# Kernel optimization log

Hardware: AMD Instinct MI355X
Metric: run time of the kernel (lower is better)

## Reference

```python
import jax, jax.numpy as jnp
import numpy as np

N_USER = 27094
M_SPOT = 42852
N_EDGE = 2_000_000
D_FEAT = 128


def setup_inputs() -> dict:
    key = jax.random.key(0)
    k1, k2, k3, k4 = jax.random.split(key, 4)
    spot_x = jax.random.normal(k1, (M_SPOT, D_FEAT), dtype=jnp.float32)
    user_x = jax.random.normal(k2, (N_USER, D_FEAT), dtype=jnp.float32)
    u_idx = jax.random.randint(k3, (N_EDGE,), 0, N_USER, dtype=jnp.int32)
    s_idx = jax.random.randint(k4, (N_EDGE,), 0, M_SPOT, dtype=jnp.int32)
    user_spot = jnp.stack([u_idx, s_idx], axis=0)  # [2, E]
    return {"spot_x": spot_x, "user_x": user_x, "user_spot": user_spot}


def reference(spot_x, user_x, user_spot):
    u = user_spot[0]  # [E] user index per edge
    s = user_spot[1]  # [E] spot index per edge
    # symmetric GCN normalization: 1/sqrt(deg_u * deg_s) per edge
    user_deg = jnp.bincount(u, length=N_USER)
    spot_deg = jnp.bincount(s, length=M_SPOT)
    div = jnp.sqrt((user_deg[u] * spot_deg[s]).astype(spot_x.dtype))[:, None]  # [E,1]
    # spot -> user aggregation
    source_spot = spot_x[s] / div                                   # [E, D]
    user_out = jax.ops.segment_sum(source_spot, u, num_segments=N_USER)
    # user -> spot aggregation
    source_user = user_x[u] / div                                   # [E, D]
    spot_out = jax.ops.segment_sum(source_user, s, num_segments=M_SPOT)
    return (spot_out, user_out)
```

## Files before the change

kernel.cpp:

```cpp
#include <hip/hip_runtime.h>
#include <stdint.h>


#define NPB_LOG2 6
#define NPB 64
#define MAXB 768
#define PART_CHUNK 2048
#define BH_CHUNK 16384
#define SORT_CAP 8192
#define RCAP 4096

__device__ __forceinline__ ushort f2bf(float f) {
    uint32_t u = __float_as_uint(f);
    return (ushort)((u + 0x7fffu + ((u >> 16) & 1u)) >> 16);
}

__global__ __launch_bounds__(256) void bhist_kernel(
        const int* __restrict__ u, const int* __restrict__ s, int E,
        int nbu, int nbs, int* __restrict__ bd) {
    __shared__ int hist[2 * MAXB];
    const int tid = threadIdx.x;
    const int nb = nbu + nbs;
    const int beg = blockIdx.x * BH_CHUNK;
    const int end = min(beg + BH_CHUNK, E);
    for (int b = tid; b < nb; b += 256) hist[b] = 0;
    __syncthreads();
    for (int i = beg + tid; i < end; i += 256) {
        atomicAdd(&hist[u[i] >> NPB_LOG2], 1);
        atomicAdd(&hist[nbu + (s[i] >> NPB_LOG2)], 1);
    }
    __syncthreads();
    for (int b = tid; b < nb; b += 256) {
        int h = hist[b];
        if (h) atomicAdd(&bd[b], h);
    }
}

__global__ __launch_bounds__(1024) void scan2_kernel(
        const int* __restrict__ bd, int nbu, int nbs,
        int* __restrict__ buoff, int* __restrict__ bsoff,
        int* __restrict__ gcu, int* __restrict__ gcs) {
    __shared__ int wsums[16];
    __shared__ int total;
    const int tid = threadIdx.x, lane = tid & 63, wid = tid >> 6;
    const int n   = blockIdx.x ? nbs : nbu;
    const int* in = blockIdx.x ? (bd + nbu) : bd;
    int* out = blockIdx.x ? bsoff : buoff;
    int* gc  = blockIdx.x ? gcs   : gcu;
    int v = (tid < n) ? in[tid] : 0;
    int x = v;
#pragma unroll
    for (int d = 1; d < 64; d <<= 1) {
        int t = __shfl_up(x, d);
        if (lane >= d) x += t;
    }
    if (lane == 63) wsums[wid] = x;
    __syncthreads();
    if (tid == 0) {
        int run = 0;
#pragma unroll
        for (int w = 0; w < 16; ++w) { int t = wsums[w]; wsums[w] = run; run += t; }
        total = run;
    }
    __syncthreads();
    int excl = wsums[wid] + (x - v);
    if (tid < n) { out[tid] = excl; gc[tid] = excl; }
    if (tid == 0) out[n] = total;
}

__global__ void convert2_kernel(const float* __restrict__ spot_x,
                                const float* __restrict__ user_x,
                                const float* __restrict__ isd_s,
                                const float* __restrict__ isd_u,
                                ushort* __restrict__ xbs, ushort* __restrict__ xbu,
                                int M, int N) {
    int idx = blockIdx.x * blockDim.x + threadIdx.x;
    if (idx >= ((M + N) << 6)) return;
    int row = idx >> 6, c = idx & 63;
    const float* x; float w; ushort* xb;
    if (row < M) { x = spot_x + ((size_t)row << 7); w = isd_s[row]; xb = xbs + ((size_t)row << 7); }
    else { row -= M; x = user_x + ((size_t)row << 7); w = isd_u[row]; xb = xbu + ((size_t)row << 7); }
    ushort2 o;
    o.x = f2bf(x[c] * w);
    o.y = f2bf(x[c + 64] * w);
    *reinterpret_cast<ushort2*>(xb + 2 * c) = o;
}

__global__ void convert_kernel(const float* __restrict__ x, const float* __restrict__ isd,
                               ushort* __restrict__ xb, int n_rows) {
    int idx = blockIdx.x * blockDim.x + threadIdx.x;
    if (idx >= (n_rows << 6)) return;
    int row = idx >> 6, c = idx & 63;
    float w = isd[row];
    const float* xr = x + ((size_t)row << 7);
    ushort2 o;
    o.x = f2bf(xr[c] * w);
    o.y = f2bf(xr[c + 64] * w);
    *reinterpret_cast<ushort2*>(xb + ((size_t)row << 7) + 2 * c) = o;
}

__global__ __launch_bounds__(256) void part2_kernel(
        const int* __restrict__ u, const int* __restrict__ s, int E,
        int nbu, int nbs, int* __restrict__ gcu, int* __restrict__ gcs,
        uint32_t* __restrict__ outU, uint32_t* __restrict__ outS) {
    __shared__ int histU[MAXB], loffU[MAXB], gbaseU[MAXB], curU[MAXB];
    __shared__ int histS[MAXB], loffS[MAXB], gbaseS[MAXB], curS[MAXB];
    __shared__ int wsum[4];
    __shared__ uint32_t sbufU[PART_CHUNK];
    __shared__ uint32_t sbufS[PART_CHUNK];
    const int tid = threadIdx.x;
    const int lane = tid & 63;
    const int wid = tid >> 6;
    const int beg = blockIdx.x * PART_CHUNK;
    const int end = min(beg + PART_CHUNK, E);
    const int cnt_total = end - beg;
    for (int b = tid; b < nbu; b += 256) histU[b] = 0;
    for (int b = tid; b < nbs; b += 256) histS[b] = 0;
    __syncthreads();
    for (int i = beg + tid; i < end; i += 256) {
        atomicAdd(&histU[u[i] >> NPB_LOG2], 1);
        atomicAdd(&histS[s[i] >> NPB_LOG2], 1);
    }
    __syncthreads();
    for (int dir = 0; dir < 2; ++dir) {
        int nb = dir ? nbs : nbu;
        int* hist = dir ? histS : histU;
        int* loff = dir ? loffS : loffU;
        int b0 = tid * 3;
        int h0 = (b0 + 0 < nb) ? hist[b0 + 0] : 0;
        int h1 = (b0 + 1 < nb) ? hist[b0 + 1] : 0;
        int h2 = (b0 + 2 < nb) ? hist[b0 + 2] : 0;
        int tsum = h0 + h1 + h2;
        int x = tsum;
#pragma unroll
        for (int d = 1; d < 64; d <<= 1) {
            int t = __shfl_up(x, d);
            if (lane >= d) x += t;
        }
        if (lane == 63) wsum[wid] = x;
        __syncthreads();
        if (tid == 0) {
            int run = 0;
#pragma unroll
            for (int w = 0; w < 4; ++w) { int t = wsum[w]; wsum[w] = run; run += t; }
        }
        __syncthreads();
        int base = wsum[wid] + (x - tsum);
        if (b0 + 0 < nb) loff[b0 + 0] = base;
        if (b0 + 1 < nb) loff[b0 + 1] = base + h0;
        if (b0 + 2 < nb) loff[b0 + 2] = base + h0 + h1;
        __syncthreads();
    }
    for (int b = tid; b < nbu; b += 256) {
        curU[b] = loffU[b];
        int c = histU[b];
        gbaseU[b] = c > 0 ? atomicAdd(&gcu[b], c) : 0;
    }
    for (int b = tid; b < nbs; b += 256) {
        curS[b] = loffS[b];
        int c = histS[b];
        gbaseS[b] = c > 0 ? atomicAdd(&gcs[b], c) : 0;
    }
    __syncthreads();
    for (int i = beg + tid; i < end; i += 256) {
        int uu = u[i], ss = s[i];
        int lu = atomicAdd(&curU[uu >> NPB_LOG2], 1);
        sbufU[lu] = ((uint32_t)uu << 16) | (uint32_t)ss;
        int ls = atomicAdd(&curS[ss >> NPB_LOG2], 1);
        sbufS[ls] = ((uint32_t)ss << 16) | (uint32_t)uu;
    }
    __syncthreads();
    for (int k = tid; k < cnt_total; k += 256) {
        uint32_t p = sbufU[k];
        int b = (int)(p >> (16 + NPB_LOG2));
        outU[gbaseU[b] + (k - loffU[b])] = p;
        uint32_t q = sbufS[k];
        int b2 = (int)(q >> (16 + NPB_LOG2));
        outS[gbaseS[b2] + (k - loffS[b2])] = q;
    }
}

__global__ __launch_bounds__(256) void bdeg2_kernel(
        const uint32_t* __restrict__ bufU, const uint32_t* __restrict__ bufS,
        const int* __restrict__ buoff, const int* __restrict__ bsoff, int nbu,
        float* __restrict__ isd_u, float* __restrict__ isd_s, int N, int M) {
    __shared__ int hist[NPB];
    const int tid = threadIdx.x;
    const int b = blockIdx.x;
    const uint32_t* buf; const int* boff; float* isd; int n_rows; int bb;
    if (b < nbu) { buf = bufU; boff = buoff; isd = isd_u; n_rows = N; bb = b; }
    else         { buf = bufS; boff = bsoff; isd = isd_s; n_rows = M; bb = b - nbu; }
    const int jbeg = boff[bb];
    const int cnt = boff[bb + 1] - jbeg;
    if (tid < NPB) hist[tid] = 0;
    __syncthreads();
    for (int k = tid; k < cnt; k += 256)
        atomicAdd(&hist[(buf[jbeg + k] >> 16) & (NPB - 1)], 1);
    __syncthreads();
    if (tid < NPB) {
        int node = (bb << NPB_LOG2) + tid;
        if (node < n_rows) {
            int h = hist[tid];
            isd[node] = h > 0 ? rsqrtf((float)h) : 0.f;
        }
    }
}

__global__ __launch_bounds__(512) void fscan3_kernel(
        const ushort* __restrict__ xb, const uint32_t* __restrict__ buf,
        const int* __restrict__ boff, const float* __restrict__ isd,
        float* __restrict__ out, int split) {
    __shared__ ushort srt[RCAP];
    __shared__ int hist[NPB];
    __shared__ int scur[NPB];
    const int tid = threadIdx.x;
    const int bucket = blockIdx.x / split;
    const int sub = blockIdx.x - bucket * split;
    const int jb = boff[bucket];
    const int cnt = boff[bucket + 1] - jb;
    if (cnt <= 0) return;
    const int sbeg = jb + (int)((long long)cnt * sub / split);
    const int send = jb + (int)((long long)cnt * (sub + 1) / split);
    const int scnt = send - sbeg;
    if (scnt <= 0) return;
    const int wid = tid >> 6, lane = tid & 63;
    const int rowbase = bucket << NPB_LOG2;

#define ROWX(sv) (*reinterpret_cast<const uint32_t*>( \
        xb + (((size_t)(sv)) << 7) + (lane << 1)))
#define UPX(rv) __uint_as_float((rv) << 16)
#define UPY(rv) __uint_as_float((rv) & 0xffff0000u)

    if (scnt <= RCAP) {
        if (tid < NPB) hist[tid] = 0;
        __syncthreads();
        uint32_t ereg[8];
#pragma unroll
        for (int k = 0; k < 8; ++k) {
            int idx = sbeg + (k << 9) + tid;
            if (idx < send) {
                ereg[k] = buf[idx];
                atomicAdd(&hist[(ereg[k] >> 16) & (NPB - 1)], 1);
            } else ereg[k] = 0u;
        }
        __syncthreads();
        if (tid < NPB) {
            int h = hist[tid];
            int x = h;
#pragma unroll
            for (int d = 1; d < 64; d <<= 1) {
                int t = __shfl_up(x, d);
                if (tid >= d) x += t;
            }
            scur[tid] = x - h;
        }
        __syncthreads();
#pragma unroll
        for (int k = 0; k < 8; ++k) {
            int idx = sbeg + (k << 9) + tid;
            if (idx < send) {
                uint32_t p = ereg[k];
                int slot = atomicAdd(&scur[(p >> 16) & (NPB - 1)], 1);
                srt[slot] = (ushort)p;
            }
        }
        __syncthreads();
        for (int ld = wid; ld < NPB; ld += 8) {
            const int deg = hist[ld];
            if (!deg) continue;
            const int off0 = scur[ld] - deg;
            float ax = 0.f, ay = 0.f;
            int j = 0;
            if (deg >= 16) {
                ushort c0 = srt[off0+0], c1 = srt[off0+1], c2 = srt[off0+2], c3 = srt[off0+3],
                       c4 = srt[off0+4], c5 = srt[off0+5], c6 = srt[off0+6], c7 = srt[off0+7];
                uint32_t r0 = ROWX(c0), r1 = ROWX(c1), r2 = ROWX(c2), r3 = ROWX(c3),
                         r4 = ROWX(c4), r5 = ROWX(c5), r6 = ROWX(c6), r7 = ROWX(c7);
                for (j = 8; j + 8 <= deg; j += 8) {
                    const int q = off0 + j;
                    ushort n0 = srt[q+0], n1 = srt[q+1], n2 = srt[q+2], n3 = srt[q+3],
                           n4 = srt[q+4], n5 = srt[q+5], n6 = srt[q+6], n7 = srt[q+7];
                    uint32_t s0 = ROWX(n0), s1 = ROWX(n1), s2 = ROWX(n2), s3 = ROWX(n3),
                             s4 = ROWX(n4), s5 = ROWX(n5), s6 = ROWX(n6), s7 = ROWX(n7);
                    ax += ((UPX(r0) + UPX(r1)) + (UPX(r2) + UPX(r3)))
                        + ((UPX(r4) + UPX(r5)) + (UPX(r6) + UPX(r7)));
                    ay += ((UPY(r0) + UPY(r1)) + (UPY(r2) + UPY(r3)))
                        + ((UPY(r4) + UPY(r5)) + (UPY(r6) + UPY(r7)));
                    r0 = s0; r1 = s1; r2 = s2; r3 = s3;
                    r4 = s4; r5 = s5; r6 = s6; r7 = s7;
                }
                ax += ((UPX(r0) + UPX(r1)) + (UPX(r2) + UPX(r3)))
                    + ((UPX(r4) + UPX(r5)) + (UPX(r6) + UPX(r7)));
                ay += ((UPY(r0) + UPY(r1)) + (UPY(r2) + UPY(r3)))
                    + ((UPY(r4) + UPY(r5)) + (UPY(r6) + UPY(r7)));
            }
            for (; j < deg; ++j) {
                uint32_t r = ROWX(srt[off0 + j]);
                ax += UPX(r); ay += UPY(r);
            }
            const float w = isd[rowbase + ld];
            const size_t ro = ((size_t)(rowbase + ld)) << 7;
            unsafeAtomicAdd(out + ro + lane,      ax * w);
            unsafeAtomicAdd(out + ro + 64 + lane, ay * w);
        }
    } else {
        const int cs = (scnt + 7) >> 3;
        const int beg = sbeg + wid * cs;
        const int end = min(beg + cs, send);
        if (beg >= end) return;
        float ax = 0.f, ay = 0.f;
        int curd = (int)(buf[beg] >> 16);
        for (int k = beg; k < end; ++k) {
            uint32_t p = buf[k];
            int d_ = (int)(p >> 16);
            if (d_ != curd) {
                float w_ = isd[curd];
                unsafeAtomicAdd(out + ((size_t)curd << 7) + lane, ax * w_);
                unsafeAtomicAdd(out + ((size_t)curd << 7) + 64 + lane, ay * w_);
                ax = 0.f; ay = 0.f; curd = d_;
            }
            uint32_t r = ROWX((ushort)p);
            ax += UPX(r); ay += UPY(r);
        }
        float w_ = isd[curd];
        unsafeAtomicAdd(out + ((size_t)curd << 7) + lane, ax * w_);
        unsafeAtomicAdd(out + ((size_t)curd << 7) + 64 + lane, ay * w_);
    }
#undef UPY
#undef UPX
#undef ROWX
}


__global__ __launch_bounds__(256) void bdeg_kernel(
        const uint32_t* __restrict__ buf, const int* __restrict__ boff,
        float* __restrict__ isd, int n_rows) {
    __shared__ int hist[NPB];
    const int tid = threadIdx.x;
    const int jbeg = boff[blockIdx.x];
    const int cnt = boff[blockIdx.x + 1] - jbeg;
    if (tid < NPB) hist[tid] = 0;
    __syncthreads();
    for (int k = tid; k < cnt; k += 256)
        atomicAdd(&hist[(buf[jbeg + k] >> 16) & (NPB - 1)], 1);
    __syncthreads();
    if (tid < NPB) {
        int node = (blockIdx.x << NPB_LOG2) + tid;
        if (node < n_rows) {
            int h = hist[tid];
            isd[node] = h > 0 ? rsqrtf((float)h) : 0.f;
        }
    }
}

__global__ __launch_bounds__(512) void fscan_kernel(
        const ushort* __restrict__ xb, const uint32_t* __restrict__ buf,
        const int* __restrict__ boff, float* __restrict__ isd_out,
        float* __restrict__ out, int n_rows) {
    __shared__ uint32_t sorted[SORT_CAP];
    __shared__ int hist[NPB];
    __shared__ int scur[NPB];
    __shared__ float isdl[NPB];
    const int tid = threadIdx.x;
    const int jbeg = boff[blockIdx.x];
    const int cnt = boff[blockIdx.x + 1] - jbeg;
    if (cnt <= 0) {
        if (tid < NPB) {
            int node = (blockIdx.x << NPB_LOG2) + tid;
            if (node < n_rows) isd_out[node] = 0.f;
        }
        return;
    }
    const bool fits = (cnt <= SORT_CAP);
    if (tid < NPB) hist[tid] = 0;
    __syncthreads();
    for (int k = tid; k < cnt; k += 512)
        atomicAdd(&hist[(buf[jbeg + k] >> 16) & (NPB - 1)], 1);
    __syncthreads();
    if (tid < NPB) {
        int h = hist[tid];
        int x = h;
#pragma unroll
        for (int d = 1; d < 64; d <<= 1) {
            int t = __shfl_up(x, d);
            if (tid >= d) x += t;
        }
        scur[tid] = x - h;
        float iv = h > 0 ? rsqrtf((float)h) : 0.f;
        isdl[tid] = iv;
        int node = (blockIdx.x << NPB_LOG2) + tid;
        if (node < n_rows) isd_out[node] = iv;
    }
    __syncthreads();
    if (fits) {
        for (int k = tid; k < cnt; k += 512) {
            uint32_t p = buf[jbeg + k];
            int slot = atomicAdd(&scur[(p >> 16) & (NPB - 1)], 1);
            sorted[slot] = p;
        }
    }
    __syncthreads();
    const int wid = tid >> 6, lane = tid & 63;
    const int cs = (cnt + 7) >> 3;
    const int beg = wid * cs;
    const int end = min(beg + cs, cnt);
    if (beg >= end) return;

#define QLD(i) (fits ? sorted[i] : buf[jbeg + (i)])
#define ROW(pv) (*reinterpret_cast<const uint32_t*>( \
        xb + (((size_t)((pv) & 0xffffu)) << 7) + (lane << 1)))
#define UPX(rv) __uint_as_float((rv) << 16)
#define UPY(rv) __uint_as_float((rv) & 0xffff0000u)
    float ax = 0.f, ay = 0.f;
    int curd = (int)(QLD(beg) >> 16);
    for (int k = beg; k < end; ++k) {
        uint32_t p = QLD(k);
        int d_ = (int)(p >> 16);
        if (d_ != curd) {
            float w_ = isdl[curd & (NPB - 1)];
            unsafeAtomicAdd(out + ((size_t)curd << 7) + lane, ax * w_);
            unsafeAtomicAdd(out + ((size_t)curd << 7) + 64 + lane, ay * w_);
            ax = 0.f; ay = 0.f; curd = d_;
        }
        uint32_t r = ROW(p);
        ax += UPX(r); ay += UPY(r);
    }
    float w_ = isdl[curd & (NPB - 1)];
    unsafeAtomicAdd(out + ((size_t)curd << 7) + lane, ax * w_);
    unsafeAtomicAdd(out + ((size_t)curd << 7) + 64 + lane, ay * w_);
#undef UPY
#undef UPX
#undef ROW
#undef QLD
}


__global__ void deg_kernel(const int* __restrict__ u, const int* __restrict__ s,
                           int E, int* __restrict__ udeg, int* __restrict__ sdeg) {
    int i = blockIdx.x * blockDim.x + threadIdx.x;
    if (i < E) {
        atomicAdd(&udeg[u[i]], 1);
        atomicAdd(&sdeg[s[i]], 1);
    }
}

__global__ void init_isd_kernel(const int* __restrict__ udeg, const int* __restrict__ sdeg,
                                float* __restrict__ isd_u, float* __restrict__ isd_s,
                                int n_user, int m_spot) {
    int i = blockIdx.x * blockDim.x + threadIdx.x;
    if (i < n_user) { int d = udeg[i]; isd_u[i] = d > 0 ? rsqrtf((float)d) : 0.f; }
    if (i < m_spot) { int d = sdeg[i]; isd_s[i] = d > 0 ? rsqrtf((float)d) : 0.f; }
}

__global__ __launch_bounds__(256) void scatter_kernel(const float* __restrict__ spot_x,
                                                      const float* __restrict__ user_x,
                                                      const int* __restrict__ u,
                                                      const int* __restrict__ s, int E,
                                                      const float* __restrict__ isd_u,
                                                      const float* __restrict__ isd_s,
                                                      float* __restrict__ spot_out,
                                                      float* __restrict__ user_out) {
    const int lane = threadIdx.x & 63;
    const int e = blockIdx.x * 4 + (threadIdx.x >> 6);
    if (e >= E) return;
    const int uu = u[e], ss = s[e];
    const float w = isd_u[uu] * isd_s[ss];
    const float2 sv = *reinterpret_cast<const float2*>(spot_x + (size_t)ss * 128 + lane * 2);
    const float2 uv = *reinterpret_cast<const float2*>(user_x + (size_t)uu * 128 + lane * 2);
    atomicAdd(&user_out[(size_t)uu * 128 + lane * 2 + 0], sv.x * w);
    atomicAdd(&user_out[(size_t)uu * 128 + lane * 2 + 1], sv.y * w);
    atomicAdd(&spot_out[(size_t)ss * 128 + lane * 2 + 0], uv.x * w);
    atomicAdd(&spot_out[(size_t)ss * 128 + lane * 2 + 1], uv.y * w);
}

static inline char* align256(char* p) {
    return (char*)(((uintptr_t)p + 255u) & ~(uintptr_t)255u);
}

extern "C" void kernel_launch(void* const* d_in, const int* in_sizes, int n_in,
                              void* d_out, int out_size, void* d_ws, size_t ws_size,
                              hipStream_t stream) {
    const float* spot_x = (const float*)d_in[0];
    const float* user_x = (const float*)d_in[1];
    const int*   edges  = (const int*)d_in[2];
    const int M = in_sizes[0] / 128;
    const int N = in_sizes[1] / 128;
    const int E = in_sizes[2] / 2;
    const int* u = edges;
    const int* s = edges + E;
    float* spot_out = (float*)d_out;
    float* user_out = (float*)d_out + (size_t)M * 128;

    const int nbu = (N + NPB - 1) / NPB;
    const int nbs = (M + NPB - 1) / NPB;
    const int nm = (N > M) ? N : M;
    const int gpart = (E + PART_CHUNK - 1) / PART_CHUNK;

    char* ws = (char*)d_ws;
    float*    isd_u = (float*)ws; ws = align256(ws + sizeof(float) * (size_t)N);
    float*    isd_s = (float*)ws; ws = align256(ws + sizeof(float) * (size_t)M);
    int*      bd    = (int*)ws;   ws = align256(ws + sizeof(int) * (size_t)(nbu + nbs));
    int*      buoff = (int*)ws;   ws = align256(ws + sizeof(int) * (size_t)(nbu + 1));
    int*      bsoff = (int*)ws;   ws = align256(ws + sizeof(int) * (size_t)(nbs + 1));
    int*      gcu   = (int*)ws;   ws = align256(ws + sizeof(int) * (size_t)nbu);
    int*      gcs   = (int*)ws;   ws = align256(ws + sizeof(int) * (size_t)nbs);
    uint32_t* bufU  = (uint32_t*)ws; ws = align256(ws + sizeof(uint32_t) * (size_t)E);
    uint32_t* bufS  = (uint32_t*)ws; ws = align256(ws + sizeof(uint32_t) * (size_t)E);
    ushort*   xbs   = (ushort*)ws;
    ushort*   xbu   = (ushort*)align256((char*)xbs + sizeof(ushort) * ((size_t)M * 128));
    size_t tierA_needed = (size_t)((char*)xbu - (char*)d_ws)
                        + sizeof(ushort) * ((size_t)N * 128);
    size_t tierB_needed = (size_t)((char*)xbs - (char*)d_ws)
                        + sizeof(ushort) * ((size_t)nm * 128);

    if (tierB_needed <= ws_size && nbu <= MAXB && nbs <= MAXB) {
        hipMemsetAsync(bd, 0, sizeof(int) * (size_t)(nbu + nbs), stream);
        hipMemsetAsync(d_out, 0, sizeof(float) * (size_t)out_size, stream);
        bhist_kernel<<<(E + BH_CHUNK - 1) / BH_CHUNK, 256, 0, stream>>>(
            u, s, E, nbu, nbs, bd);
        scan2_kernel<<<2, 1024, 0, stream>>>(bd, nbu, nbs, buoff, bsoff, gcu, gcs);
        part2_kernel<<<gpart, 256, 0, stream>>>(u, s, E, nbu, nbs, gcu, gcs, bufU, bufS);
        if (tierA_needed <= ws_size) {
            bdeg2_kernel<<<nbu + nbs, 256, 0, stream>>>(
                bufU, bufS, buoff, bsoff, nbu, isd_u, isd_s, N, M);
            convert2_kernel<<<(((M + N) << 6) + 255) / 256, 256, 0, stream>>>(
                spot_x, user_x, isd_s, isd_u, xbs, xbu, M, N);
            int splitU = 2048 / nbu; if (splitU < 1) splitU = 1; if (splitU > 16) splitU = 16;
            int splitS = 2048 / nbs; if (splitS < 1) splitS = 1; if (splitS > 16) splitS = 16;
            fscan3_kernel<<<nbu * splitU, 512, 0, stream>>>(
                xbs, bufU, buoff, isd_u, user_out, splitU);
            fscan3_kernel<<<nbs * splitS, 512, 0, stream>>>(
                xbu, bufS, bsoff, isd_s, spot_out, splitS);
        } else {
            ushort* xb = xbs;
            bdeg_kernel<<<nbs, 256, 0, stream>>>(bufS, bsoff, isd_s, M);
            convert_kernel<<<((M << 6) + 255) / 256, 256, 0, stream>>>(spot_x, isd_s, xb, M);
            fscan_kernel<<<nbu, 512, 0, stream>>>(xb, bufU, buoff, isd_u, user_out, N);
            convert_kernel<<<((N << 6) + 255) / 256, 256, 0, stream>>>(user_x, isd_u, xb, N);
            fscan_kernel<<<nbs, 512, 0, stream>>>(xb, bufS, bsoff, isd_s, spot_out, M);
        }
        return;
    }

    {
        char* w2 = (char*)d_ws;
        int*   udeg2  = (int*)w2;   w2 += sizeof(int) * (size_t)N;
        int*   sdeg2  = (int*)w2;   w2 += sizeof(int) * (size_t)M;
        float* isd_u2 = (float*)w2; w2 += sizeof(float) * (size_t)N;
        float* isd_s2 = (float*)w2; w2 += sizeof(float) * (size_t)M;
        if ((size_t)(w2 - (char*)d_ws) <= ws_size) {
            hipMemsetAsync(udeg2, 0, sizeof(int) * (size_t)(N + M), stream);
            deg_kernel<<<(E + 255) / 256, 256, 0, stream>>>(u, s, E, udeg2, sdeg2);
            init_isd_kernel<<<(nm + 255) / 256, 256, 0, stream>>>(
                udeg2, sdeg2, isd_u2, isd_s2, N, M);
            hipMemsetAsync(d_out, 0, sizeof(float) * (size_t)out_size, stream);
            scatter_kernel<<<((size_t)E + 3) / 4, 256, 0, stream>>>(
                spot_x, user_x, u, s, E, isd_u2, isd_s2, spot_out, user_out);
        }
    }
}
```

Measured before the change: 293.6 us.

## Fully sort bucket edges in place, then gather with fixed-chunk wave scans

```diff
diff --git a/kernel.cpp b/kernel.cpp
--- a/kernel.cpp
+++ b/kernel.cpp
@@ -8,7 +8,7 @@
 #define PART_CHUNK 2048
 #define BH_CHUNK 16384
 #define SORT_CAP 8192
-#define RCAP 4096
+#define CSCAN_CH 256
 
 __device__ __forceinline__ ushort f2bf(float f) {
     uint32_t u = __float_as_uint(f);
@@ -180,202 +180,28 @@
     }
 }
 
-__global__ __launch_bounds__(256) void bdeg2_kernel(
-        const uint32_t* __restrict__ bufU, const uint32_t* __restrict__ bufS,
+__global__ __launch_bounds__(256) void bsort3b_kernel(
+        uint32_t* __restrict__ bufU, uint32_t* __restrict__ bufS,
         const int* __restrict__ buoff, const int* __restrict__ bsoff, int nbu,
         float* __restrict__ isd_u, float* __restrict__ isd_s, int N, int M) {
+    __shared__ uint32_t stage[SORT_CAP];
     __shared__ int hist[NPB];
+    __shared__ int cur[NPB];
     const int tid = threadIdx.x;
     const int b = blockIdx.x;
-    const uint32_t* buf; const int* boff; float* isd; int n_rows; int bb;
+    uint32_t* buf; const int* boff; float* isd; int n_rows; int bb;
     if (b < nbu) { buf = bufU; boff = buoff; isd = isd_u; n_rows = N; bb = b; }
     else         { buf = bufS; boff = bsoff; isd = isd_s; n_rows = M; bb = b - nbu; }
     const int jbeg = boff[bb];
     const int cnt = boff[bb + 1] - jbeg;
-    if (tid < NPB) hist[tid] = 0;
-    __syncthreads();
-    for (int k = tid; k < cnt; k += 256)
-        atomicAdd(&hist[(buf[jbeg + k] >> 16) & (NPB - 1)], 1);
-    __syncthreads();
-    if (tid < NPB) {
-        int node = (bb << NPB_LOG2) + tid;
-        if (node < n_rows) {
-            int h = hist[tid];
-            isd[node] = h > 0 ? rsqrtf((float)h) : 0.f;
-        }
-    }
-}
-
-__global__ __launch_bounds__(512) void fscan3_kernel(
-        const ushort* __restrict__ xb, const uint32_t* __restrict__ buf,
-        const int* __restrict__ boff, const float* __restrict__ isd,
-        float* __restrict__ out, int split) {
-    __shared__ ushort srt[RCAP];
-    __shared__ int hist[NPB];
-    __shared__ int scur[NPB];
-    const int tid = threadIdx.x;
-    const int bucket = blockIdx.x / split;
-    const int sub = blockIdx.x - bucket * split;
-    const int jb = boff[bucket];
-    const int cnt = boff[bucket + 1] - jb;
-    if (cnt <= 0) return;
-    const int sbeg = jb + (int)((long long)cnt * sub / split);
-    const int send = jb + (int)((long long)cnt * (sub + 1) / split);
-    const int scnt = send - sbeg;
-    if (scnt <= 0) return;
-    const int wid = tid >> 6, lane = tid & 63;
-    const int rowbase = bucket << NPB_LOG2;
-
-#define ROWX(sv) (*reinterpret_cast<const uint32_t*>( \
-        xb + (((size_t)(sv)) << 7) + (lane << 1)))
-#define UPX(rv) __uint_as_float((rv) << 16)
-#define UPY(rv) __uint_as_float((rv) & 0xffff0000u)
-
-    if (scnt <= RCAP) {
-        if (tid < NPB) hist[tid] = 0;
-        __syncthreads();
-        uint32_t ereg[8];
-#pragma unroll
-        for (int k = 0; k < 8; ++k) {
-            int idx = sbeg + (k << 9) + tid;
-            if (idx < send) {
-                ereg[k] = buf[idx];
-                atomicAdd(&hist[(ereg[k] >> 16) & (NPB - 1)], 1);
-            } else ereg[k] = 0u;
-        }
-        __syncthreads();
-        if (tid < NPB) {
-            int h = hist[tid];
-            int x = h;
-#pragma unroll
-            for (int d = 1; d < 64; d <<= 1) {
-                int t = __shfl_up(x, d);
-                if (tid >= d) x += t;
-            }
-            scur[tid] = x - h;
-        }
-        __syncthreads();
-#pragma unroll
-        for (int k = 0; k < 8; ++k) {
-            int idx = sbeg + (k << 9) + tid;
-            if (idx < send) {
-                uint32_t p = ereg[k];
-                int slot = atomicAdd(&scur[(p >> 16) & (NPB - 1)], 1);
-                srt[slot] = (ushort)p;
-            }
-        }
-        __syncthreads();
-        for (int ld = wid; ld < NPB; ld += 8) {
-            const int deg = hist[ld];
-            if (!deg) continue;
-            const int off0 = scur[ld] - deg;
-            float ax = 0.f, ay = 0.f;
-            int j = 0;
-            if (deg >= 16) {
-                ushort c0 = srt[off0+0], c1 = srt[off0+1], c2 = srt[off0+2], c3 = srt[off0+3],
-                       c4 = srt[off0+4], c5 = srt[off0+5], c6 = srt[off0+6], c7 = srt[off0+7];
-                uint32_t r0 = ROWX(c0), r1 = ROWX(c1), r2 = ROWX(c2), r3 = ROWX(c3),
-                         r4 = ROWX(c4), r5 = ROWX(c5), r6 = ROWX(c6), r7 = ROWX(c7);
-                for (j = 8; j + 8 <= deg; j += 8) {
-                    const int q = off0 + j;
-                    ushort n0 = srt[q+0], n1 = srt[q+1], n2 = srt[q+2], n3 = srt[q+3],
-                           n4 = srt[q+4], n5 = srt[q+5], n6 = srt[q+6], n7 = srt[q+7];
-                    uint32_t s0 = ROWX(n0), s1 = ROWX(n1), s2 = ROWX(n2), s3 = ROWX(n3),
-                             s4 = ROWX(n4), s5 = ROWX(n5), s6 = ROWX(n6), s7 = ROWX(n7);
-                    ax += ((UPX(r0) + UPX(r1)) + (UPX(r2) + UPX(r3)))
-                        + ((UPX(r4) + UPX(r5)) + (UPX(r6) + UPX(r7)));
-                    ay += ((UPY(r0) + UPY(r1)) + (UPY(r2) + UPY(r3)))
-                        + ((UPY(r4) + UPY(r5)) + (UPY(r6) + UPY(r7)));
-                    r0 = s0; r1 = s1; r2 = s2; r3 = s3;
-                    r4 = s4; r5 = s5; r6 = s6; r7 = s7;
-                }
-                ax += ((UPX(r0) + UPX(r1)) + (UPX(r2) + UPX(r3)))
-                    + ((UPX(r4) + UPX(r5)) + (UPX(r6) + UPX(r7)));
-                ay += ((UPY(r0) + UPY(r1)) + (UPY(r2) + UPY(r3)))
-                    + ((UPY(r4) + UPY(r5)) + (UPY(r6) + UPY(r7)));
-            }
-            for (; j < deg; ++j) {
-                uint32_t r = ROWX(srt[off0 + j]);
-                ax += UPX(r); ay += UPY(r);
-            }
-            const float w = isd[rowbase + ld];
-            const size_t ro = ((size_t)(rowbase + ld)) << 7;
-            unsafeAtomicAdd(out + ro + lane,      ax * w);
-            unsafeAtomicAdd(out + ro + 64 + lane, ay * w);
-        }
-    } else {
-        const int cs = (scnt + 7) >> 3;
-        const int beg = sbeg + wid * cs;
-        const int end = min(beg + cs, send);
-        if (beg >= end) return;
-        float ax = 0.f, ay = 0.f;
-        int curd = (int)(buf[beg] >> 16);
-        for (int k = beg; k < end; ++k) {
-            uint32_t p = buf[k];
-            int d_ = (int)(p >> 16);
-            if (d_ != curd) {
-                float w_ = isd[curd];
-                unsafeAtomicAdd(out + ((size_t)curd << 7) + lane, ax * w_);
-                unsafeAtomicAdd(out + ((size_t)curd << 7) + 64 + lane, ay * w_);
-                ax = 0.f; ay = 0.f; curd = d_;
-            }
-            uint32_t r = ROWX((ushort)p);
-            ax += UPX(r); ay += UPY(r);
-        }
-        float w_ = isd[curd];
-        unsafeAtomicAdd(out + ((size_t)curd << 7) + lane, ax * w_);
-        unsafeAtomicAdd(out + ((size_t)curd << 7) + 64 + lane, ay * w_);
-    }
-#undef UPY
-#undef UPX
-#undef ROWX
-}
-
-
-__global__ __launch_bounds__(256) void bdeg_kernel(
-        const uint32_t* __restrict__ buf, const int* __restrict__ boff,
-        float* __restrict__ isd, int n_rows) {
-    __shared__ int hist[NPB];
-    const int tid = threadIdx.x;
-    const int jbeg = boff[blockIdx.x];
-    const int cnt = boff[blockIdx.x + 1] - jbeg;
-    if (tid < NPB) hist[tid] = 0;
-    __syncthreads();
-    for (int k = tid; k < cnt; k += 256)
-        atomicAdd(&hist[(buf[jbeg + k] >> 16) & (NPB - 1)], 1);
-    __syncthreads();
-    if (tid < NPB) {
-        int node = (blockIdx.x << NPB_LOG2) + tid;
-        if (node < n_rows) {
-            int h = hist[tid];
-            isd[node] = h > 0 ? rsqrtf((float)h) : 0.f;
-        }
-    }
-}
-
-__global__ __launch_bounds__(512) void fscan_kernel(
-        const ushort* __restrict__ xb, const uint32_t* __restrict__ buf,
-        const int* __restrict__ boff, float* __restrict__ isd_out,
-        float* __restrict__ out, int n_rows) {
-    __shared__ uint32_t sorted[SORT_CAP];
-    __shared__ int hist[NPB];
-    __shared__ int scur[NPB];
-    __shared__ float isdl[NPB];
-    const int tid = threadIdx.x;
-    const int jbeg = boff[blockIdx.x];
-    const int cnt = boff[blockIdx.x + 1] - jbeg;
-    if (cnt <= 0) {
-        if (tid < NPB) {
-            int node = (blockIdx.x << NPB_LOG2) + tid;
-            if (node < n_rows) isd_out[node] = 0.f;
-        }
-        return;
-    }
     const bool fits = (cnt <= SORT_CAP);
     if (tid < NPB) hist[tid] = 0;
     __syncthreads();
-    for (int k = tid; k < cnt; k += 512)
-        atomicAdd(&hist[(buf[jbeg + k] >> 16) & (NPB - 1)], 1);
+    for (int k = tid; k < cnt; k += 256) {
+        uint32_t p = buf[jbeg + k];
+        if (fits) stage[k] = p;
+        atomicAdd(&hist[(p >> 16) & (NPB - 1)], 1);
+    }
     __syncthreads();
     if (tid < NPB) {
         int h = hist[tid];
@@ -385,53 +211,91 @@
             int t = __shfl_up(x, d);
             if (tid >= d) x += t;
         }
-        scur[tid] = x - h;
-        float iv = h > 0 ? rsqrtf((float)h) : 0.f;
-        isdl[tid] = iv;
-        int node = (blockIdx.x << NPB_LOG2) + tid;
-        if (node < n_rows) isd_out[node] = iv;
+        cur[tid] = x - h;
+        int node = (bb << NPB_LOG2) + tid;
+        if (node < n_rows) isd[node] = h > 0 ? rsqrtf((float)h) : 0.f;
     }
     __syncthreads();
     if (fits) {
-        for (int k = tid; k < cnt; k += 512) {
-            uint32_t p = buf[jbeg + k];
-            int slot = atomicAdd(&scur[(p >> 16) & (NPB - 1)], 1);
-            sorted[slot] = p;
-        }
-    }
-    __syncthreads();
-    const int wid = tid >> 6, lane = tid & 63;
-    const int cs = (cnt + 7) >> 3;
-    const int beg = wid * cs;
-    const int end = min(beg + cs, cnt);
-    if (beg >= end) return;
-
-#define QLD(i) (fits ? sorted[i] : buf[jbeg + (i)])
+        for (int k = tid; k < cnt; k += 256) {
+            uint32_t p = stage[k];
+            int slot = atomicAdd(&cur[(p >> 16) & (NPB - 1)], 1);
+            buf[jbeg + slot] = p;
+        }
+    }
+}
+
+__global__ __launch_bounds__(256) void cscan_kernel(
+        const ushort* __restrict__ xb, const uint32_t* __restrict__ packed, int E,
+        const float* __restrict__ isd, float* __restrict__ out) {
+    const int lane = threadIdx.x & 63;
+    const int wave = (blockIdx.x << 2) + (threadIdx.x >> 6);
+    const int base = wave * CSCAN_CH;
+    if (base >= E) return;
+    const int n = min(CSCAN_CH, E - base);
+    const uint32_t* pp = packed + base;
+    float ax = 0.f, ay = 0.f;
+    int cur = (int)(pp[0] >> 16);
+
 #define ROW(pv) (*reinterpret_cast<const uint32_t*>( \
         xb + (((size_t)((pv) & 0xffffu)) << 7) + (lane << 1)))
 #define UPX(rv) __uint_as_float((rv) << 16)
 #define UPY(rv) __uint_as_float((rv) & 0xffff0000u)
-    float ax = 0.f, ay = 0.f;
-    int curd = (int)(QLD(beg) >> 16);
-    for (int k = beg; k < end; ++k) {
-        uint32_t p = QLD(k);
-        int d_ = (int)(p >> 16);
-        if (d_ != curd) {
-            float w_ = isdl[curd & (NPB - 1)];
-            unsafeAtomicAdd(out + ((size_t)curd << 7) + lane, ax * w_);
-            unsafeAtomicAdd(out + ((size_t)curd << 7) + 64 + lane, ay * w_);
-            ax = 0.f; ay = 0.f; curd = d_;
-        }
+#define FLUSH() do { float w_ = isd[cur];                                  \
+        unsafeAtomicAdd(out + ((size_t)cur << 7) + lane, ax * w_);         \
+        unsafeAtomicAdd(out + ((size_t)cur << 7) + 64 + lane, ay * w_);    \
+        ax = 0.f; ay = 0.f; } while (0)
+#define PROC(pv, rv) do { int d_ = (int)((pv) >> 16);                      \
+        if (d_ != cur) { FLUSH(); cur = d_; }                              \
+        ax += UPX(rv); ay += UPY(rv); } while (0)
+#define GRP8(Aa, Ab, r0, r1, r2, r3, r4, r5, r6, r7) do {                  \
+    if ((((Aa.x ^ Ab.w) >> 16) == 0) && ((int)(Aa.x >> 16) == cur)) {      \
+        float sx = ((UPX(r0) + UPX(r1)) + (UPX(r2) + UPX(r3)))             \
+                 + ((UPX(r4) + UPX(r5)) + (UPX(r6) + UPX(r7)));            \
+        float sy = ((UPY(r0) + UPY(r1)) + (UPY(r2) + UPY(r3)))             \
+                 + ((UPY(r4) + UPY(r5)) + (UPY(r6) + UPY(r7)));            \
+        ax += sx; ay += sy;                                                \
+    } else {                                                               \
+        PROC(Aa.x, r0); PROC(Aa.y, r1); PROC(Aa.z, r2); PROC(Aa.w, r3);    \
+        PROC(Ab.x, r4); PROC(Ab.y, r5); PROC(Ab.z, r6); PROC(Ab.w, r7);    \
+    } } while (0)
+
+    int k = 0;
+    if (n >= 24) {
+        uint4 P0a = *(const uint4*)(pp + 0),  P0b = *(const uint4*)(pp + 4);
+        uint4 P1a = *(const uint4*)(pp + 8),  P1b = *(const uint4*)(pp + 12);
+        uint32_t a0 = ROW(P0a.x), a1 = ROW(P0a.y), a2 = ROW(P0a.z), a3 = ROW(P0a.w),
+                 a4 = ROW(P0b.x), a5 = ROW(P0b.y), a6 = ROW(P0b.z), a7 = ROW(P0b.w);
+        uint4 P2a = *(const uint4*)(pp + 16), P2b = *(const uint4*)(pp + 20);
+        uint32_t b0 = ROW(P1a.x), b1 = ROW(P1a.y), b2 = ROW(P1a.z), b3 = ROW(P1a.w),
+                 b4 = ROW(P1b.x), b5 = ROW(P1b.y), b6 = ROW(P1b.z), b7 = ROW(P1b.w);
+        for (k = 24; k + 8 <= n; k += 8) {
+            uint4 P3a = *(const uint4*)(pp + k), P3b = *(const uint4*)(pp + k + 4);
+            uint32_t c0 = ROW(P2a.x), c1 = ROW(P2a.y), c2 = ROW(P2a.z), c3 = ROW(P2a.w),
+                     c4 = ROW(P2b.x), c5 = ROW(P2b.y), c6 = ROW(P2b.z), c7 = ROW(P2b.w);
+            GRP8(P0a, P0b, a0, a1, a2, a3, a4, a5, a6, a7);
+            P0a = P1a; P0b = P1b; P1a = P2a; P1b = P2b; P2a = P3a; P2b = P3b;
+            a0 = b0; a1 = b1; a2 = b2; a3 = b3; a4 = b4; a5 = b5; a6 = b6; a7 = b7;
+            b0 = c0; b1 = c1; b2 = c2; b3 = c3; b4 = c4; b5 = c5; b6 = c6; b7 = c7;
+        }
+        uint32_t c0 = ROW(P2a.x), c1 = ROW(P2a.y), c2 = ROW(P2a.z), c3 = ROW(P2a.w),
+                 c4 = ROW(P2b.x), c5 = ROW(P2b.y), c6 = ROW(P2b.z), c7 = ROW(P2b.w);
+        GRP8(P0a, P0b, a0, a1, a2, a3, a4, a5, a6, a7);
+        GRP8(P1a, P1b, b0, b1, b2, b3, b4, b5, b6, b7);
+        GRP8(P2a, P2b, c0, c1, c2, c3, c4, c5, c6, c7);
+    }
+    for (; k < n; ++k) {
+        uint32_t p = pp[k];
         uint32_t r = ROW(p);
-        ax += UPX(r); ay += UPY(r);
-    }
-    float w_ = isdl[curd & (NPB - 1)];
-    unsafeAtomicAdd(out + ((size_t)curd << 7) + lane, ax * w_);
-    unsafeAtomicAdd(out + ((size_t)curd << 7) + 64 + lane, ay * w_);
+        PROC(p, r);
+    }
+    FLUSH();
+#undef GRP8
+#undef PROC
+#undef FLUSH
 #undef UPY
 #undef UPX
 #undef ROW
-#undef QLD
 }
 
 
@@ -495,6 +359,7 @@
     const int nbs = (M + NPB - 1) / NPB;
     const int nm = (N > M) ? N : M;
     const int gpart = (E + PART_CHUNK - 1) / PART_CHUNK;
+    const int gscan = ((E + CSCAN_CH - 1) / CSCAN_CH + 3) / 4;
 
     char* ws = (char*)d_ws;
     float*    isd_u = (float*)ws; ws = align256(ws + sizeof(float) * (size_t)N);
@@ -520,24 +385,19 @@
             u, s, E, nbu, nbs, bd);
         scan2_kernel<<<2, 1024, 0, stream>>>(bd, nbu, nbs, buoff, bsoff, gcu, gcs);
         part2_kernel<<<gpart, 256, 0, stream>>>(u, s, E, nbu, nbs, gcu, gcs, bufU, bufS);
+        bsort3b_kernel<<<nbu + nbs, 256, 0, stream>>>(
+            bufU, bufS, buoff, bsoff, nbu, isd_u, isd_s, N, M);
         if (tierA_needed <= ws_size) {
-            bdeg2_kernel<<<nbu + nbs, 256, 0, stream>>>(
-                bufU, bufS, buoff, bsoff, nbu, isd_u, isd_s, N, M);
             convert2_kernel<<<(((M + N) << 6) + 255) / 256, 256, 0, stream>>>(
                 spot_x, user_x, isd_s, isd_u, xbs, xbu, M, N);
-            int splitU = 2048 / nbu; if (splitU < 1) splitU = 1; if (splitU > 16) splitU = 16;
-            int splitS = 2048 / nbs; if (splitS < 1) splitS = 1; if (splitS > 16) splitS = 16;
-            fscan3_kernel<<<nbu * splitU, 512, 0, stream>>>(
-                xbs, bufU, buoff, isd_u, user_out, splitU);
-            fscan3_kernel<<<nbs * splitS, 512, 0, stream>>>(
-                xbu, bufS, bsoff, isd_s, spot_out, splitS);
+            cscan_kernel<<<gscan, 256, 0, stream>>>(xbs, bufU, E, isd_u, user_out);
+            cscan_kernel<<<gscan, 256, 0, stream>>>(xbu, bufS, E, isd_s, spot_out);
         } else {
             ushort* xb = xbs;
-            bdeg_kernel<<<nbs, 256, 0, stream>>>(bufS, bsoff, isd_s, M);
             convert_kernel<<<((M << 6) + 255) / 256, 256, 0, stream>>>(spot_x, isd_s, xb, M);
-            fscan_kernel<<<nbu, 512, 0, stream>>>(xb, bufU, buoff, isd_u, user_out, N);
+            cscan_kernel<<<gscan, 256, 0, stream>>>(xb, bufU, E, isd_u, user_out);
             convert_kernel<<<((N << 6) + 255) / 256, 256, 0, stream>>>(user_x, isd_u, xb, N);
-            fscan_kernel<<<nbs, 512, 0, stream>>>(xb, bufS, bsoff, isd_s, spot_out, M);
+            cscan_kernel<<<gscan, 256, 0, stream>>>(xb, bufS, E, isd_s, spot_out);
         }
         return;
     }
```

New measurement: 238.3 us. 1.23x faster.
